# Kernel tuning notes

Hardware: AMD Instinct MI355X
Metric: run time of the kernel (lower is better)

## Reference

```python
import jax, jax.numpy as jnp
import numpy as np

NUM_NODES = 50000
NUM_EDGES = 800000
HIDDEN = 128
HEADS = 8
HEAD_DIM = HIDDEN // HEADS  # 16
FF_HIDDEN = 4 * HIDDEN
LN_EPS = 1e-5


def _xavier(key, shape, gain=0.01):
    fan_out, fan_in = shape
    bound = gain * np.sqrt(6.0 / (fan_in + fan_out))
    return jax.random.uniform(key, shape, jnp.float32, -bound, bound)


def setup_inputs() -> dict:
    key = jax.random.key(0)
    ks = jax.random.split(key, 10)
    x = jax.random.normal(ks[0], (NUM_NODES, HIDDEN), jnp.float32)
    edge_index = jax.random.randint(ks[1], (2, NUM_EDGES), 0, NUM_NODES, jnp.int64)
    return {
        "x": x,
        "edge_index": edge_index,
        "Wq": _xavier(ks[2], (HIDDEN, HIDDEN)),
        "bq": jnp.zeros((HIDDEN,), jnp.float32),
        "Wk": _xavier(ks[3], (HIDDEN, HIDDEN)),
        "bk": jnp.zeros((HIDDEN,), jnp.float32),
        "Wv": _xavier(ks[4], (HIDDEN, HIDDEN)),
        "bv": jnp.zeros((HIDDEN,), jnp.float32),
        "Wo": _xavier(ks[5], (HIDDEN, HIDDEN)),
        "bo": jnp.zeros((HIDDEN,), jnp.float32),
        "W1": _xavier(ks[6], (FF_HIDDEN, HIDDEN)),
        "b1": jnp.zeros((FF_HIDDEN,), jnp.float32),
        "W2": _xavier(ks[7], (HIDDEN, FF_HIDDEN)),
        "b2": jnp.zeros((HIDDEN,), jnp.float32),
        "g1": jnp.ones((HIDDEN,), jnp.float32),
        "be1": jnp.zeros((HIDDEN,), jnp.float32),
        "g2": jnp.ones((HIDDEN,), jnp.float32),
        "be2": jnp.zeros((HIDDEN,), jnp.float32),
    }


def _layernorm(v, g, b):
    mu = jnp.mean(v, axis=-1, keepdims=True)
    var = jnp.mean(jnp.square(v - mu), axis=-1, keepdims=True)
    return (v - mu) * jax.lax.rsqrt(var + LN_EPS) * g + b


def _forward(x, edge_index, Wq, bq, Wk, bk, Wv, bv, Wo, bo, W1, b1, W2, b2, g1, be1, g2, be2):
    src = edge_index[0]  # key/value side (_j)
    dst = edge_index[1]  # query side (_i), aggregation index
    scale = 1.0 / np.sqrt(HEAD_DIM)

    # Euclidean manifold: GeometricLinear == plain linear
    q = (x @ Wq.T + bq).reshape(NUM_NODES, HEADS, HEAD_DIM)
    k = (x @ Wk.T + bk).reshape(NUM_NODES, HEADS, HEAD_DIM)
    v = (x @ Wv.T + bv).reshape(NUM_NODES, HEADS, HEAD_DIM)

    # per-edge attention scores [E, H]
    alpha = jnp.einsum('ehd,ehd->eh', q[dst], k[src]) * scale
    # segment softmax over destination nodes
    m = jax.ops.segment_max(alpha, dst, num_segments=NUM_NODES)  # [N, H]
    ea = jnp.exp(alpha - m[dst])
    denom = jax.ops.segment_sum(ea, dst, num_segments=NUM_NODES)  # [N, H]
    alpha = ea / (denom[dst] + 1e-16)

    # scatter-add weighted values -> [N, H, D]
    agg = jax.ops.segment_sum(v[src] * alpha[..., None], dst, num_segments=NUM_NODES)
    att = agg.reshape(NUM_NODES, HIDDEN) @ Wo.T + bo

    # residual + norm1 (Euclidean)
    h = _layernorm(x + att, g1, be1)

    # feed-forward: fc1 -> exact GELU -> fc2
    ff = (jax.nn.gelu(h @ W1.T + b1, approximate=False)) @ W2.T + b2

    # residual + norm2
    return _layernorm(h + ff, g2, be2)


def reference(x, edge_index, Wq, bq, Wk, bk, Wv, bv, Wo, bo, W1, b1, W2, b2, g1, be1, g2, be2):
    return _forward(x, edge_index, Wq, bq, Wk, bk, Wv, bv, Wo, bo, W1, b1, W2, b2, g1, be1, g2, be2)
```

## Files before the change

kernel.cpp:

```cpp
#include <hip/hip_runtime.h>
#include <math.h>

#define N_HEADS 8
#define HEAD_DIM 16
#define HID 128
#define QKV_ROWB 512

typedef unsigned short ushort_t;
typedef __attribute__((ext_vector_type(8))) short short8;
typedef __attribute__((ext_vector_type(4))) float floatx4;
typedef __attribute__((ext_vector_type(2))) float f32x2;

#define KV_SCALE 64.0f
#define KV_INV_SCALE 0.015625f

#define W2_SCALE 65536.0f
#define A1_SCALE 512.0f
#define FF2_DESCALE (1.0f / 33554432.0f)

#define COUNT_BLOCKS 2048
#define SCAT_BLOCKS 2048

__device__ __forceinline__ ushort_t f2bf(float f) {
    unsigned u = __float_as_uint(f);
    unsigned r = (u + 0x7FFFu + ((u >> 16) & 1u)) >> 16;
    return (ushort_t)r;
}
__device__ __forceinline__ float bf2f(ushort_t u) {
    return __uint_as_float(((unsigned)u) << 16);
}

__device__ __forceinline__ float gelu_f(float x) {
    float z = fabsf(x) * 0.70710678118654752f;
    float t = 1.0f / (1.0f + 0.3275911f * z);
    float y = t * (0.254829592f + t * (-0.284496736f + t * (1.421413741f
            + t * (-1.453152027f + t * 1.061405429f))));
    float e = 1.0f - y * __expf(-z * z);
    e = copysignf(e, x);
    return 0.5f * x * (1.0f + e);
}

__global__ __launch_bounds__(256)
void prep_count_kernel(const float* __restrict__ x,
                 const float* __restrict__ Wq, const float* __restrict__ Wk,
                 const float* __restrict__ Wv, const float* __restrict__ Wo,
                 const float* __restrict__ W1, const float* __restrict__ W2,
                 const float* __restrict__ bq, const float* __restrict__ bk,
                 const float* __restrict__ bv,
                 const int* __restrict__ dst, int* __restrict__ cnt,
                 int* __restrict__ rank, int E, int N,
                 ushort_t* __restrict__ xfrag, ushort_t* __restrict__ wofrag,
                 ushort_t* __restrict__ wqkvf,
                 ushort_t* __restrict__ w1frag,
                 unsigned char* __restrict__ w2frag8,
                 float* __restrict__ bqkv, int xchunks)
{
    if (blockIdx.x < COUNT_BLOCKS) {
        int coh = blockIdx.x & 7;
        int bc  = blockIdx.x >> 3;
        int rr  = (N + 7) >> 3;
        int nlo = coh * rr;
        int nhi = nlo + rr; if (nhi > N) nhi = N;
        const int stride = (COUNT_BLOCKS >> 3) * 256;
        for (int e = bc * 256 + threadIdx.x; e < E; e += stride) {
            int d = dst[e];
            if (d >= nlo && d < nhi) rank[e] = atomicAdd(&cnt[d], 1);
        }
        return;
    }
    int i = (blockIdx.x - COUNT_BLOCKS) * 256 + threadIdx.x;
    if (i < xchunks) {
        int t16 = i >> 8;
        int rem = i & 255;
        int lane = rem & 63;
        int row = t16 * 16 + (lane & 15);
        int k   = (rem >> 6) * 32 + (lane >> 4) * 8;
        const float* s = x + (size_t)row * HID + k;
        short8 v;
#pragma unroll
        for (int e = 0; e < 8; ++e) v[e] = (short)f2bf(s[e]);
        *(short8*)(xfrag + (size_t)i * 8) = v;
        return;
    }
    int j = i - xchunks;
    if (j < 2048) {
        int lane = j & 63, tk = j >> 6;
        int t16 = tk >> 2, kst = tk & 3;
        int row = t16 * 16 + (lane & 15);
        int kb  = kst * 32 + (lane >> 4) * 8;
        const float* s = Wo + (size_t)row * HID + kb;
        short8 v;
#pragma unroll
        for (int e = 0; e < 8; ++e) v[e] = (short)f2bf(s[e]);
        *(short8*)(wofrag + (size_t)j * 8) = v;
        return;
    }
    int b = j - 2048;
    if (b < 6144) {
        int w = b >> 11;
        int rem = b & 2047;
        int t16 = rem >> 8;
        int rem2 = rem & 255;
        int lane = rem2 & 63;
        int row = t16 * 16 + (lane & 15);
        int k   = ((rem2 >> 6) & 3) * 32 + (lane >> 4) * 8;
        const float* W = (w == 0) ? Wq : (w == 1) ? Wk : Wv;
        const float* s = W + (size_t)row * HID + k;
        short8 v;
#pragma unroll
        for (int e = 0; e < 8; ++e) v[e] = (short)f2bf(s[e]);
        *(short8*)(wqkvf + (size_t)b * 8) = v;
        return;
    }
    int c = b - 6144;
    if (c < 8192) {
        int lane = c & 63, tk = c >> 6;
        int t16 = tk >> 2, kst = tk & 3;
        int row = t16 * 16 + (lane & 15);
        int kb  = kst * 32 + (lane >> 4) * 8;
        const float* s = W1 + (size_t)row * HID + kb;
        short8 v;
#pragma unroll
        for (int e = 0; e < 8; ++e) v[e] = (short)f2bf(s[e]);
        *(short8*)(w1frag + (size_t)c * 8) = v;
        return;
    }
    int c2 = c - 8192;
    if (c2 < 8192) {
        int lane = c2 & 63, tk = c2 >> 6;
        int t16 = tk >> 4, kst = tk & 15;
        int row = t16 * 16 + (lane & 15);
        int kb  = kst * 32 + (lane >> 4) * 8;
        const float* s = W2 + (size_t)row * 512 + kb;
        unsigned u0 = 0, u1 = 0;
        u0 = __builtin_amdgcn_cvt_pk_fp8_f32(s[0]*W2_SCALE, s[1]*W2_SCALE, u0, false);
        u0 = __builtin_amdgcn_cvt_pk_fp8_f32(s[2]*W2_SCALE, s[3]*W2_SCALE, u0, true);
        u1 = __builtin_amdgcn_cvt_pk_fp8_f32(s[4]*W2_SCALE, s[5]*W2_SCALE, u1, false);
        u1 = __builtin_amdgcn_cvt_pk_fp8_f32(s[6]*W2_SCALE, s[7]*W2_SCALE, u1, true);
        uint2 o; o.x = u0; o.y = u1;
        *(uint2*)(w2frag8 + (size_t)c2 * 8) = o;
        return;
    }
    int d = c2 - 8192;
    if (d < 384) {
        bqkv[d] = (d < 128) ? bq[d] : (d < 256) ? bk[d - 128] : bv[d - 256];
    }
}

__global__ __launch_bounds__(256)
void scan1_kernel(const int* __restrict__ cnt, int* __restrict__ parts, int N)
{
    __shared__ int sd[256];
    int t = threadIdx.x;
    int base = blockIdx.x * 1024 + t * 4;
    int s = 0;
#pragma unroll
    for (int j = 0; j < 4; ++j) if (base + j < N) s += cnt[base + j];
    sd[t] = s; __syncthreads();
    for (int off = 128; off; off >>= 1) {
        if (t < off) sd[t] += sd[t + off];
        __syncthreads();
    }
    if (t == 0) parts[blockIdx.x] = sd[0];
}

__global__ __launch_bounds__(256)
void scan2_kernel(const int* __restrict__ parts, int* __restrict__ poff, int nb)
{
    __shared__ int sd[256];
    int t = threadIdx.x;
    int v = (t < nb) ? parts[t] : 0;
    sd[t] = v; __syncthreads();
    for (int off = 1; off < 256; off <<= 1) {
        int u = (t >= off) ? sd[t - off] : 0;
        __syncthreads();
        sd[t] += u;
        __syncthreads();
    }
    if (t < nb) poff[t] = sd[t] - v;
}

__global__ __launch_bounds__(256)
void scan3_kernel(const int* __restrict__ cnt, const int* __restrict__ poff,
                  int* __restrict__ rp, int N)
{
    __shared__ int sd[256];
    int t = threadIdx.x;
    int base = blockIdx.x * 1024 + t * 4;
    int v0 = (base + 0 < N) ? cnt[base + 0] : 0;
    int v1 = (base + 1 < N) ? cnt[base + 1] : 0;
    int v2 = (base + 2 < N) ? cnt[base + 2] : 0;
    int v3 = (base + 3 < N) ? cnt[base + 3] : 0;
    int s = v0 + v1 + v2 + v3;
    sd[t] = s; __syncthreads();
    for (int off = 1; off < 256; off <<= 1) {
        int u = (t >= off) ? sd[t - off] : 0;
        __syncthreads();
        sd[t] += u;
        __syncthreads();
    }
    int o = poff[blockIdx.x] + sd[t] - s;
    if (base + 0 < N) rp[base + 0] = o;
    if (base + 1 < N) rp[base + 1] = o + v0;
    if (base + 2 < N) rp[base + 2] = o + v0 + v1;
    if (base + 3 < N) rp[base + 3] = o + v0 + v1 + v2;
}

__global__ __launch_bounds__(256)
void scatter_qkv_kernel(const int* __restrict__ src, const int* __restrict__ dst,
                 const int* __restrict__ rp, const int* __restrict__ rank,
                 int* __restrict__ ssrc, int E, int N,
                 const ushort_t* __restrict__ xfrag,
                 const ushort_t* __restrict__ wqkvf,
                 const float* __restrict__ bqkv,
                 ushort_t* __restrict__ qkvb, int nt16, int nxq)
{
    __shared__ __align__(16) ushort_t sT[4][16 * 136];

    if (blockIdx.x < SCAT_BLOCKS) {
        int coh = blockIdx.x & 7;
        int bc  = blockIdx.x >> 3;
        int rr  = (N + 7) >> 3;
        int nlo = coh * rr;
        int nhi = nlo + rr; if (nhi > N) nhi = N;
        const int stride = (SCAT_BLOCKS >> 3) * 256;
        for (int e = bc * 256 + threadIdx.x; e < E; e += stride) {
            int d = dst[e];
            if (d >= nlo && d < nhi) ssrc[rp[d] + rank[e]] = src[e];
        }
        return;
    }

    const int qi = blockIdx.x - SCAT_BLOCKS;
    const int y  = qi / nxq;
    const int bx = qi - y * nxq;
    const int wave = threadIdx.x >> 6, lane = threadIdx.x & 63;
    const int l15 = lane & 15, l4 = lane >> 4;
    const int gt0 = bx * 8 + wave * 2;
    const int gt0c = (gt0 < nt16) ? gt0 : nt16 - 1;
    const int gt1c = (gt0 + 1 < nt16) ? gt0 + 1 : nt16 - 1;

    floatx4 acc[2][8];
#pragma unroll
    for (int i = 0; i < 2; ++i)
#pragma unroll
        for (int j = 0; j < 8; ++j) acc[i][j] = (floatx4)(0.f);

    const ushort_t* wf = wqkvf + (size_t)y * 16384;
#pragma unroll
    for (int kst = 0; kst < 4; ++kst) {
        short8 a0 = *(const short8*)&xfrag[(((size_t)gt0c * 4 + kst) * 64 + lane) * 8];
        short8 a1 = *(const short8*)&xfrag[(((size_t)gt1c * 4 + kst) * 64 + lane) * 8];
        short8 bv[8];
#pragma unroll
        for (int j = 0; j < 8; ++j)
            bv[j] = *(const short8*)&wf[(((size_t)j * 4 + kst) * 64 + lane) * 8];
#pragma unroll
        for (int j = 0; j < 8; ++j) {
            acc[0][j] = __builtin_amdgcn_mfma_f32_16x16x32_bf16(a0, bv[j], acc[0][j], 0, 0, 0);
            acc[1][j] = __builtin_amdgcn_mfma_f32_16x16x32_bf16(a1, bv[j], acc[1][j], 0, 0, 0);
        }
    }

    float bb[8];
#pragma unroll
    for (int j = 0; j < 8; ++j) bb[j] = bqkv[y * 128 + j * 16 + l15];

#pragma unroll
    for (int i = 0; i < 2; ++i) {
        const int gt = gt0 + i;
#pragma unroll
        for (int j = 0; j < 8; ++j)
#pragma unroll
            for (int r = 0; r < 4; ++r) {
                float v = acc[i][j][r] + bb[j];
                if (y) v *= KV_SCALE;
                sT[wave][(l4 * 4 + r) * 136 + j * 16 + l15] = f2bf(v);
            }
        if (gt < nt16) {
            if (y == 0) {
#pragma unroll
                for (int c = 0; c < 4; ++c) {
                    int ch = l4 * 4 + c;
                    *(short8*)&qkvb[(size_t)(gt * 16 + l15) * 256 + ch * 8] =
                        *(const short8*)&sT[wave][l15 * 136 + ch * 8];
                }
            } else {
                const int koff = (y - 1) * 8;
#pragma unroll
                for (int c = 0; c < 4; ++c) {
                    int ch = l4 * 4 + c;
                    short8 s = *(const short8*)&sT[wave][l15 * 136 + ch * 8];
                    unsigned u0 = 0, u1 = 0;
                    u0 = __builtin_amdgcn_cvt_pk_fp8_f32(
                             bf2f((ushort_t)s[0]), bf2f((ushort_t)s[1]), u0, false);
                    u0 = __builtin_amdgcn_cvt_pk_fp8_f32(
                             bf2f((ushort_t)s[2]), bf2f((ushort_t)s[3]), u0, true);
                    u1 = __builtin_amdgcn_cvt_pk_fp8_f32(
                             bf2f((ushort_t)s[4]), bf2f((ushort_t)s[5]), u1, false);
                    u1 = __builtin_amdgcn_cvt_pk_fp8_f32(
                             bf2f((ushort_t)s[6]), bf2f((ushort_t)s[7]), u1, true);
                    uint2 o; o.x = u0; o.y = u1;
                    *(uint2*)((char*)qkvb + (size_t)(gt * 16 + l15) * QKV_ROWB
                              + 256 + ch * 16 + koff) = o;
                }
            }
        }
    }
}

__global__ __launch_bounds__(256)
void wow_kernel(const ushort_t* __restrict__ aggfrag,
                const ushort_t* __restrict__ wofrag,
                const float* __restrict__ bo,
                const float* __restrict__ x,
                const float* __restrict__ g, const float* __restrict__ be,
                ushort_t* __restrict__ hb, ushort_t* __restrict__ hfrag, int M)
{
    __shared__ __align__(16) ushort_t sT[4][16 * 136];
    const int wave = threadIdx.x >> 6, lane = threadIdx.x & 63;
    const int t32 = blockIdx.x * 4 + wave;
    const int nt32 = (M + 31) / 32;
    if (t32 >= nt32) return;
    const int nt16 = (M + 15) / 16;
    const int gt0 = t32 * 2;
    const int gt1c = (gt0 + 1 < nt16) ? gt0 + 1 : nt16 - 1;
    const int l15 = lane & 15, l4 = lane >> 4;

    floatx4 acc[2][8];
#pragma unroll
    for (int i = 0; i < 2; ++i)
#pragma unroll
        for (int j = 0; j < 8; ++j) acc[i][j] = (floatx4)(0.f);

#pragma unroll
    for (int kst = 0; kst < 4; ++kst) {
        short8 a0 = *(const short8*)&aggfrag[(((size_t)gt0  * 4 + kst) * 64 + lane) * 8];
        short8 a1 = *(const short8*)&aggfrag[(((size_t)gt1c * 4 + kst) * 64 + lane) * 8];
        short8 bv[8];
#pragma unroll
        for (int j = 0; j < 8; ++j)
            bv[j] = *(const short8*)&wofrag[(((size_t)j * 4 + kst) * 64 + lane) * 8];
#pragma unroll
        for (int j = 0; j < 8; ++j) {
            acc[0][j] = __builtin_amdgcn_mfma_f32_16x16x32_bf16(a0, bv[j], acc[0][j], 0, 0, 0);
            acc[1][j] = __builtin_amdgcn_mfma_f32_16x16x32_bf16(a1, bv[j], acc[1][j], 0, 0, 0);
        }
    }

    float bov[8], gv[8], bev[8];
#pragma unroll
    for (int j = 0; j < 8; ++j) {
        int oc = j * 16 + l15;
        bov[j] = bo[oc]; gv[j] = g[oc]; bev[j] = be[oc];
    }

#pragma unroll
    for (int i = 0; i < 2; ++i) {
        const int gt = gt0 + i;
        const int rb = gt * 16;
#pragma unroll
        for (int j = 0; j < 8; ++j) {
            int oc = j * 16 + l15;
#pragma unroll
            for (int r = 0; r < 4; ++r) {
                int row = rb + l4 * 4 + r;
                int rc = (row < M) ? row : M - 1;
                acc[i][j][r] += bov[j] + x[(size_t)rc * HID + oc];
            }
        }
#pragma unroll
        for (int r = 0; r < 4; ++r) {
            float s1 = 0.f, s2 = 0.f;
#pragma unroll
            for (int j = 0; j < 8; ++j) {
                s1 += acc[i][j][r];
                s2 += acc[i][j][r] * acc[i][j][r];
            }
            s1 += __shfl_xor(s1, 1); s1 += __shfl_xor(s1, 2);
            s1 += __shfl_xor(s1, 4); s1 += __shfl_xor(s1, 8);
            s2 += __shfl_xor(s2, 1); s2 += __shfl_xor(s2, 2);
            s2 += __shfl_xor(s2, 4); s2 += __shfl_xor(s2, 8);
            float mu = s1 * (1.f / 128.f);
            float var = s2 * (1.f / 128.f) - mu * mu;
            float rstd = rsqrtf(var + 1e-5f);
#pragma unroll
            for (int j = 0; j < 8; ++j) {
                float v = (acc[i][j][r] - mu) * rstd * gv[j] + bev[j];
                sT[wave][(l4 * 4 + r) * 136 + j * 16 + l15] = f2bf(v);
            }
        }
        if (gt < nt16) {
#pragma unroll
            for (int c = 0; c < 4; ++c) {
                int ch = l4 * 4 + c;
                *(short8*)&hb[(size_t)(gt * 16 + l15) * HID + ch * 8] =
                    *(const short8*)&sT[wave][l15 * 136 + ch * 8];
            }
#pragma unroll
            for (int q = 0; q < 4; ++q)
                *(short8*)&hfrag[(((size_t)gt * 4 + q) * 64 + lane) * 8] =
                    *(const short8*)&sT[wave][l15 * 136 + q * 32 + l4 * 8];
        }
    }
}

__global__ __launch_bounds__(256)
void ff1w_kernel(const ushort_t* __restrict__ hfrag,
                 const ushort_t* __restrict__ w1frag,
                 const float* __restrict__ b1,
                 unsigned char* __restrict__ a1img, int M)
{
    __shared__ __align__(16) ushort_t sT[4][16 * 136];
    const int wave = threadIdx.x >> 6, lane = threadIdx.x & 63;
    const int cg = wave;
    const int nt16 = (M + 15) / 16;
    const int gt0 = blockIdx.x * 2;
    const int gt1 = gt0 + 1;
    const int gt1c = (gt1 < nt16) ? gt1 : nt16 - 1;
    const int l15 = lane & 15, l4 = lane >> 4;

    floatx4 acc[2][8];
#pragma unroll
    for (int i = 0; i < 2; ++i)
#pragma unroll
        for (int j = 0; j < 8; ++j) acc[i][j] = (floatx4)(0.f);

#pragma unroll
    for (int kst = 0; kst < 4; ++kst) {
        short8 a0 = *(const short8*)&hfrag[(((size_t)gt0  * 4 + kst) * 64 + lane) * 8];
        short8 a1 = *(const short8*)&hfrag[(((size_t)gt1c * 4 + kst) * 64 + lane) * 8];
        short8 bv[8];
#pragma unroll
        for (int j = 0; j < 8; ++j)
            bv[j] = *(const short8*)&w1frag[((((size_t)cg * 8 + j) * 4 + kst) * 64 + lane) * 8];
#pragma unroll
        for (int j = 0; j < 8; ++j) {
            acc[0][j] = __builtin_amdgcn_mfma_f32_16x16x32_bf16(a0, bv[j], acc[0][j], 0, 0, 0);
            acc[1][j] = __builtin_amdgcn_mfma_f32_16x16x32_bf16(a1, bv[j], acc[1][j], 0, 0, 0);
        }
    }

    float b1v[8];
#pragma unroll
    for (int j = 0; j < 8; ++j) b1v[j] = b1[cg * 128 + j * 16 + l15];

#pragma unroll
    for (int i = 0; i < 2; ++i) {
        const int gt = i ? gt1 : gt0;
#pragma unroll
        for (int j = 0; j < 8; ++j)
#pragma unroll
            for (int r = 0; r < 4; ++r)
                sT[wave][(l4 * 4 + r) * 136 + j * 16 + l15] =
                    f2bf(gelu_f(acc[i][j][r] + b1v[j]));
        if (gt < nt16) {
#pragma unroll
            for (int q = 0; q < 4; ++q) {
                float v[8];
#pragma unroll
                for (int e = 0; e < 8; ++e)
                    v[e] = bf2f(sT[wave][l15 * 136 + q * 32 + l4 * 8 + e]) * A1_SCALE;
                unsigned u0 = 0, u1 = 0;
                u0 = __builtin_amdgcn_cvt_pk_fp8_f32(v[0], v[1], u0, false);
                u0 = __builtin_amdgcn_cvt_pk_fp8_f32(v[2], v[3], u0, true);
                u1 = __builtin_amdgcn_cvt_pk_fp8_f32(v[4], v[5], u1, false);
                u1 = __builtin_amdgcn_cvt_pk_fp8_f32(v[6], v[7], u1, true);
                uint2 o; o.x = u0; o.y = u1;
                *(uint2*)(a1img + (((size_t)gt * 16 + cg * 4 + q) * 64 + lane) * 8) = o;
            }
        }
    }
}

__global__ __launch_bounds__(256)
void ff2w_kernel(const unsigned char* __restrict__ a1img,
                 const unsigned char* __restrict__ w2frag8,
                 const ushort_t* __restrict__ hb,
                 const float* __restrict__ b2,
                 const float* __restrict__ g, const float* __restrict__ be,
                 float* __restrict__ out, int M)
{
    const int wave = threadIdx.x >> 6, lane = threadIdx.x & 63;
    const int t32 = blockIdx.x * 4 + wave;
    const int nt32 = (M + 31) / 32;
    if (t32 >= nt32) return;
    const int nt16 = (M + 15) / 16;
    const int gt0 = t32 * 2;
    const int gt1c = (gt0 + 1 < nt16) ? gt0 + 1 : nt16 - 1;
    const int l15 = lane & 15, l4 = lane >> 4;

    floatx4 acc[2][8];
#pragma unroll
    for (int i = 0; i < 2; ++i)
#pragma unroll
        for (int j = 0; j < 8; ++j) acc[i][j] = (floatx4)(0.f);

#pragma unroll
    for (int kst = 0; kst < 16; ++kst) {
        long a0 = *(const long*)(a1img + (((size_t)gt0  * 16 + kst) * 64 + lane) * 8);
        long a1 = *(const long*)(a1img + (((size_t)gt1c * 16 + kst) * 64 + lane) * 8);
        long bv[8];
#pragma unroll
        for (int j = 0; j < 8; ++j)
            bv[j] = *(const long*)(w2frag8 + (((size_t)j * 16 + kst) * 64 + lane) * 8);
#pragma unroll
        for (int j = 0; j < 8; ++j) {
            acc[0][j] = __builtin_amdgcn_mfma_f32_16x16x32_fp8_fp8(a0, bv[j], acc[0][j], 0, 0, 0);
            acc[1][j] = __builtin_amdgcn_mfma_f32_16x16x32_fp8_fp8(a1, bv[j], acc[1][j], 0, 0, 0);
        }
    }

    float b2v[8], gv[8], bev[8];
#pragma unroll
    for (int j = 0; j < 8; ++j) {
        int oc = j * 16 + l15;
        b2v[j] = b2[oc]; gv[j] = g[oc]; bev[j] = be[oc];
    }

#pragma unroll
    for (int i = 0; i < 2; ++i) {
        const int rb = (t32 * 2 + i) * 16;
#pragma unroll
        for (int j = 0; j < 8; ++j) {
            int oc = j * 16 + l15;
#pragma unroll
            for (int r = 0; r < 4; ++r) {
                int row = rb + l4 * 4 + r;
                int rc = (row < M) ? row : M - 1;
                acc[i][j][r] = acc[i][j][r] * FF2_DESCALE + b2v[j]
                             + bf2f(hb[(size_t)rc * HID + oc]);
            }
        }
#pragma unroll
        for (int r = 0; r < 4; ++r) {
            float s1 = 0.f, s2 = 0.f;
#pragma unroll
            for (int j = 0; j < 8; ++j) {
                s1 += acc[i][j][r];
                s2 += acc[i][j][r] * acc[i][j][r];
            }
            s1 += __shfl_xor(s1, 1); s1 += __shfl_xor(s1, 2);
            s1 += __shfl_xor(s1, 4); s1 += __shfl_xor(s1, 8);
            s2 += __shfl_xor(s2, 1); s2 += __shfl_xor(s2, 2);
            s2 += __shfl_xor(s2, 4); s2 += __shfl_xor(s2, 8);
            float mu = s1 * (1.f / 128.f);
            float var = s2 * (1.f / 128.f) - mu * mu;
            float rstd = rsqrtf(var + 1e-5f);
            int row = rb + l4 * 4 + r;
            if (row < M) {
#pragma unroll
                for (int j = 0; j < 8; ++j)
                    out[(size_t)row * HID + j * 16 + l15] =
                        (acc[i][j][r] - mu) * rstd * gv[j] + bev[j];
            }
        }
    }
}

__global__ __launch_bounds__(256)
void attn_fused_kernel(const ushort_t* __restrict__ qkvb, const int* __restrict__ rp,
                       const int* __restrict__ ssrc, ushort_t* __restrict__ aggfrag,
                       int N, int E)
{
    int wave = threadIdx.x >> 6, lane = threadIdx.x & 63;
    int n = blockIdx.x * 4 + wave;
    if (n >= N) return;
    int grp = lane >> 4;
    int cb  = (lane & 15) * 16;
    const char* base = (const char*)qkvb;

    short8 qv = *(const short8*)(base + n * QKV_ROWB + cb);
    float q[8];
#pragma unroll
    for (int j = 0; j < 8; ++j) q[j] = bf2f((ushort_t)qv[j]) * (0.25f / KV_SCALE);

    int r0 = rp[n];
    int r1 = (n + 1 < N) ? rp[n + 1] : E;
    float acc[8] = {0.f, 0.f, 0.f, 0.f, 0.f, 0.f, 0.f, 0.f};
    float l = 0.f;

    int r = r0;
    for (; r + 8 <= r1; r += 8) {
        int s0 = ssrc[r + grp];
        int s1 = ssrc[r + 4 + grp];
        uint4 kv0 = *(const uint4*)(base + s0 * QKV_ROWB + 256 + cb);
        uint4 kv1 = *(const uint4*)(base + s1 * QKV_ROWB + 256 + cb);

        f32x2 a0 = __builtin_amdgcn_cvt_pk_f32_fp8(kv0.x, false);
        f32x2 a1 = __builtin_amdgcn_cvt_pk_f32_fp8(kv0.x, true);
        f32x2 a2 = __builtin_amdgcn_cvt_pk_f32_fp8(kv0.y, false);
        f32x2 a3 = __builtin_amdgcn_cvt_pk_f32_fp8(kv0.y, true);
        f32x2 b0 = __builtin_amdgcn_cvt_pk_f32_fp8(kv1.x, false);
        f32x2 b1 = __builtin_amdgcn_cvt_pk_f32_fp8(kv1.x, true);
        f32x2 b2 = __builtin_amdgcn_cvt_pk_f32_fp8(kv1.y, false);
        f32x2 b3 = __builtin_amdgcn_cvt_pk_f32_fp8(kv1.y, true);

        float p0 = 0.f, p1 = 0.f;
        p0 = fmaf(q[0], a0.x, p0); p0 = fmaf(q[1], a0.y, p0);
        p0 = fmaf(q[2], a1.x, p0); p0 = fmaf(q[3], a1.y, p0);
        p0 = fmaf(q[4], a2.x, p0); p0 = fmaf(q[5], a2.y, p0);
        p0 = fmaf(q[6], a3.x, p0); p0 = fmaf(q[7], a3.y, p0);
        p1 = fmaf(q[0], b0.x, p1); p1 = fmaf(q[1], b0.y, p1);
        p1 = fmaf(q[2], b1.x, p1); p1 = fmaf(q[3], b1.y, p1);
        p1 = fmaf(q[4], b2.x, p1); p1 = fmaf(q[5], b2.y, p1);
        p1 = fmaf(q[6], b3.x, p1); p1 = fmaf(q[7], b3.y, p1);

        p0 += __shfl_xor(p0, 1);
        p1 += __shfl_xor(p1, 1);
        float e0 = __expf(p0), e1 = __expf(p1);
        l += e0 + e1;

        f32x2 v0 = __builtin_amdgcn_cvt_pk_f32_fp8(kv0.z, false);
        f32x2 v1 = __builtin_amdgcn_cvt_pk_f32_fp8(kv0.z, true);
        f32x2 v2 = __builtin_amdgcn_cvt_pk_f32_fp8(kv0.w, false);
        f32x2 v3 = __builtin_amdgcn_cvt_pk_f32_fp8(kv0.w, true);
        f32x2 w0 = __builtin_amdgcn_cvt_pk_f32_fp8(kv1.z, false);
        f32x2 w1 = __builtin_amdgcn_cvt_pk_f32_fp8(kv1.z, true);
        f32x2 w2 = __builtin_amdgcn_cvt_pk_f32_fp8(kv1.w, false);
        f32x2 w3 = __builtin_amdgcn_cvt_pk_f32_fp8(kv1.w, true);

        acc[0] = fmaf(e0, v0.x, acc[0]); acc[1] = fmaf(e0, v0.y, acc[1]);
        acc[2] = fmaf(e0, v1.x, acc[2]); acc[3] = fmaf(e0, v1.y, acc[3]);
        acc[4] = fmaf(e0, v2.x, acc[4]); acc[5] = fmaf(e0, v2.y, acc[5]);
        acc[6] = fmaf(e0, v3.x, acc[6]); acc[7] = fmaf(e0, v3.y, acc[7]);
        acc[0] = fmaf(e1, w0.x, acc[0]); acc[1] = fmaf(e1, w0.y, acc[1]);
        acc[2] = fmaf(e1, w1.x, acc[2]); acc[3] = fmaf(e1, w1.y, acc[3]);
        acc[4] = fmaf(e1, w2.x, acc[4]); acc[5] = fmaf(e1, w2.y, acc[5]);
        acc[6] = fmaf(e1, w3.x, acc[6]); acc[7] = fmaf(e1, w3.y, acc[7]);
    }
    for (; r < r1; r += 4) {
        int e = r + grp;
        int s = ssrc[(e < r1) ? e : r0];
        uint4 kv = *(const uint4*)(base + s * QKV_ROWB + 256 + cb);
        f32x2 a0 = __builtin_amdgcn_cvt_pk_f32_fp8(kv.x, false);
        f32x2 a1 = __builtin_amdgcn_cvt_pk_f32_fp8(kv.x, true);
        f32x2 a2 = __builtin_amdgcn_cvt_pk_f32_fp8(kv.y, false);
        f32x2 a3 = __builtin_amdgcn_cvt_pk_f32_fp8(kv.y, true);
        float p = 0.f;
        p = fmaf(q[0], a0.x, p); p = fmaf(q[1], a0.y, p);
        p = fmaf(q[2], a1.x, p); p = fmaf(q[3], a1.y, p);
        p = fmaf(q[4], a2.x, p); p = fmaf(q[5], a2.y, p);
        p = fmaf(q[6], a3.x, p); p = fmaf(q[7], a3.y, p);
        p += __shfl_xor(p, 1);
        float ea = (e < r1) ? __expf(p) : 0.f;
        l += ea;
        f32x2 v0 = __builtin_amdgcn_cvt_pk_f32_fp8(kv.z, false);
        f32x2 v1 = __builtin_amdgcn_cvt_pk_f32_fp8(kv.z, true);
        f32x2 v2 = __builtin_amdgcn_cvt_pk_f32_fp8(kv.w, false);
        f32x2 v3 = __builtin_amdgcn_cvt_pk_f32_fp8(kv.w, true);
        acc[0] = fmaf(ea, v0.x, acc[0]); acc[1] = fmaf(ea, v0.y, acc[1]);
        acc[2] = fmaf(ea, v1.x, acc[2]); acc[3] = fmaf(ea, v1.y, acc[3]);
        acc[4] = fmaf(ea, v2.x, acc[4]); acc[5] = fmaf(ea, v2.y, acc[5]);
        acc[6] = fmaf(ea, v3.x, acc[6]); acc[7] = fmaf(ea, v3.y, acc[7]);
    }

#pragma unroll
    for (int j = 0; j < 8; ++j) {
        acc[j] += __shfl_xor(acc[j], 16);
        acc[j] += __shfl_xor(acc[j], 32);
    }
    l += __shfl_xor(l, 16);
    l += __shfl_xor(l, 32);
    float inv = KV_INV_SCALE / (l + 1e-16f);
    if (grp == 0) {
        short8 o;
#pragma unroll
        for (int j = 0; j < 8; ++j) o[j] = (short)f2bf(acc[j] * inv);
        int t16 = n >> 4, kst = lane >> 2;
        int lp = (n & 15) + ((lane & 3) << 4);
        *(short8*)&aggfrag[(((size_t)t16 * 4 + kst) * 64 + lp) * 8] = o;
    }
}

extern "C" void kernel_launch(void* const* d_in, const int* in_sizes, int n_in,
                              void* d_out, int out_size, void* d_ws, size_t ws_size,
                              hipStream_t stream)
{
    const float* x  = (const float*)d_in[0];
    const int*   ei = (const int*)d_in[1];
    const float* Wq = (const float*)d_in[2];
    const float* bq = (const float*)d_in[3];
    const float* Wk = (const float*)d_in[4];
    const float* bk = (const float*)d_in[5];
    const float* Wv = (const float*)d_in[6];
    const float* bv = (const float*)d_in[7];
    const float* Wo = (const float*)d_in[8];
    const float* bo = (const float*)d_in[9];
    const float* W1 = (const float*)d_in[10];
    const float* b1 = (const float*)d_in[11];
    const float* W2 = (const float*)d_in[12];
    const float* b2 = (const float*)d_in[13];
    const float* g1 = (const float*)d_in[14];
    const float* be1= (const float*)d_in[15];
    const float* g2 = (const float*)d_in[16];
    const float* be2= (const float*)d_in[17];
    float* out = (float*)d_out;

    const int N = in_sizes[0] / HID;
    const int E = in_sizes[1] / 2;
    const int* srcp = ei;
    const int* dstp = ei + E;

    const size_t NH = (size_t)N * HID;
    float* wsf = (float*)d_ws;

    const int nt16 = (N + 15) / 16;
    const int nt32 = (N + 31) / 32;

    ushort_t* xfrag   = (ushort_t*)wsf;
    ushort_t* qkvb    = (ushort_t*)(wsf + NH / 2);
    ushort_t* hfrag   = (ushort_t*)(wsf + NH + NH / 2);
    ushort_t* aggfrag = (ushort_t*)(wsf + 2 * NH);
    ushort_t* hb      = (ushort_t*)wsf;
    unsigned char* a1img = (unsigned char*)(wsf + NH / 2);

    ushort_t* U       = (ushort_t*)(wsf + 2 * NH + NH / 2);
    ushort_t* wofrag  = U;
    ushort_t* wqkvf   = U + 16384;
    ushort_t* w1frag  = U + 65536;
    unsigned char* w2frag8 = (unsigned char*)(U + 131072);
    float*    bqkv = (float*)(w2frag8 + 65536);
    int*      rp   = (int*)(bqkv + 384);
    int*      cnt  = rp + (N + 1);
    int*      poff = cnt + N;
    int*      parts= poff + 256;
    int*      ssrc = parts + 256;
    int*      rank = ssrc + E;

    hipMemsetAsync(cnt, 0, N * sizeof(int), stream);
    const int xchunks = nt16 * 256;
    const int ptot = xchunks + 2048 + 6144 + 8192 + 8192 + 384;
    const int prepB = (ptot + 255) / 256;
    prep_count_kernel<<<COUNT_BLOCKS + prepB, 256, 0, stream>>>(
        x, Wq, Wk, Wv, Wo, W1, W2, bq, bk, bv,
        dstp, cnt, rank, E, N,
        xfrag, wofrag, wqkvf, w1frag, w2frag8, bqkv, xchunks);

    const int nb = (N + 1023) / 1024;
    scan1_kernel<<<nb, 256, 0, stream>>>(cnt, parts, N);
    scan2_kernel<<<1, 256, 0, stream>>>(parts, poff, nb);
    scan3_kernel<<<nb, 256, 0, stream>>>(cnt, poff, rp, N);

    const int nxq = (nt16 + 7) / 8;
    scatter_qkv_kernel<<<SCAT_BLOCKS + nxq * 3, 256, 0, stream>>>(
        srcp, dstp, rp, rank, ssrc, E, N,
        xfrag, wqkvf, bqkv, qkvb, nt16, nxq);

    attn_fused_kernel<<<(N + 3) / 4, 256, 0, stream>>>(
        qkvb, rp, ssrc, aggfrag, N, E);

    wow_kernel<<<(nt32 + 3) / 4, 256, 0, stream>>>(
        aggfrag, wofrag, bo, x, g1, be1, hb, hfrag, N);

    ff1w_kernel<<<nt32, 256, 0, stream>>>(hfrag, w1frag, b1, a1img, N);

    ff2w_kernel<<<(nt32 + 3) / 4, 256, 0, stream>>>(
        a1img, w2frag8, hb, b2, g2, be2, out, N);
}
```

Baseline: 298.0 us.

## Fuse output projection, LayerNorm, FFN and final LayerNorm into one kernel

Merges the Wo projection + residual + LN1 kernel, the FF1+GELU kernel and the FF2 + residual + LN2 kernel into a single per-wave kernel. Each wave keeps its 32-row tile of h in LDS, computes the 512-wide hidden layer in four 128-column chunks, quantises each chunk to fp8 in LDS and accumulates FF2 immediately. This removes the global round-trips of hb, hfrag and the fp8 activation image, plus two launches. In exchange it uses much more LDS per block and more accumulator registers, which can lower occupancy, and FF1 now runs on one wave per row tile rather than four waves sharing it.

```diff
diff --git a/kernel.cpp b/kernel.cpp
--- a/kernel.cpp
+++ b/kernel.cpp
@@ -310,14 +310,21 @@
 }
 
 __global__ __launch_bounds__(256)
-void wow_kernel(const ushort_t* __restrict__ aggfrag,
-                const ushort_t* __restrict__ wofrag,
-                const float* __restrict__ bo,
-                const float* __restrict__ x,
-                const float* __restrict__ g, const float* __restrict__ be,
-                ushort_t* __restrict__ hb, ushort_t* __restrict__ hfrag, int M)
+void ffall_kernel(const ushort_t* __restrict__ aggfrag,
+                  const ushort_t* __restrict__ wofrag,
+                  const float* __restrict__ bo,
+                  const float* __restrict__ x,
+                  const float* __restrict__ g1, const float* __restrict__ be1,
+                  const ushort_t* __restrict__ w1frag,
+                  const float* __restrict__ b1,
+                  const unsigned char* __restrict__ w2frag8,
+                  const float* __restrict__ b2,
+                  const float* __restrict__ g2, const float* __restrict__ be2,
+                  float* __restrict__ out, int M)
 {
-    __shared__ __align__(16) ushort_t sT[4][16 * 136];
+    __shared__ __align__(16) ushort_t sH[4][32 * 136];
+    __shared__ __align__(16) unsigned char sA[4][32 * 136];
+    __shared__ __align__(16) ushort_t sS[4][16 * 136];
     const int wave = threadIdx.x >> 6, lane = threadIdx.x & 63;
     const int t32 = blockIdx.x * 4 + wave;
     const int nt32 = (M + 31) / 32;
@@ -332,7 +339,6 @@
     for (int i = 0; i < 2; ++i)
 #pragma unroll
         for (int j = 0; j < 8; ++j) acc[i][j] = (floatx4)(0.f);
-
 #pragma unroll
     for (int kst = 0; kst < 4; ++kst) {
         short8 a0 = *(const short8*)&aggfrag[(((size_t)gt0  * 4 + kst) * 64 + lane) * 8];
@@ -348,211 +354,160 @@
         }
     }
 
-    float bov[8], gv[8], bev[8];
-#pragma unroll
-    for (int j = 0; j < 8; ++j) {
-        int oc = j * 16 + l15;
-        bov[j] = bo[oc]; gv[j] = g[oc]; bev[j] = be[oc];
-    }
-
-#pragma unroll
-    for (int i = 0; i < 2; ++i) {
-        const int gt = gt0 + i;
-        const int rb = gt * 16;
+    {
+        float bov[8], gv[8], bev[8];
 #pragma unroll
         for (int j = 0; j < 8; ++j) {
             int oc = j * 16 + l15;
+            bov[j] = bo[oc]; gv[j] = g1[oc]; bev[j] = be1[oc];
+        }
+#pragma unroll
+        for (int i = 0; i < 2; ++i) {
+            const int rb = (gt0 + i) * 16;
+#pragma unroll
+            for (int j = 0; j < 8; ++j) {
+                int oc = j * 16 + l15;
+#pragma unroll
+                for (int r = 0; r < 4; ++r) {
+                    int row = rb + l4 * 4 + r;
+                    int rc = (row < M) ? row : M - 1;
+                    acc[i][j][r] += bov[j] + x[(size_t)rc * HID + oc];
+                }
+            }
 #pragma unroll
             for (int r = 0; r < 4; ++r) {
-                int row = rb + l4 * 4 + r;
-                int rc = (row < M) ? row : M - 1;
-                acc[i][j][r] += bov[j] + x[(size_t)rc * HID + oc];
-            }
-        }
-#pragma unroll
-        for (int r = 0; r < 4; ++r) {
-            float s1 = 0.f, s2 = 0.f;
+                float s1 = 0.f, s2 = 0.f;
+#pragma unroll
+                for (int j = 0; j < 8; ++j) {
+                    s1 += acc[i][j][r];
+                    s2 += acc[i][j][r] * acc[i][j][r];
+                }
+                s1 += __shfl_xor(s1, 1); s1 += __shfl_xor(s1, 2);
+                s1 += __shfl_xor(s1, 4); s1 += __shfl_xor(s1, 8);
+                s2 += __shfl_xor(s2, 1); s2 += __shfl_xor(s2, 2);
+                s2 += __shfl_xor(s2, 4); s2 += __shfl_xor(s2, 8);
+                float mu = s1 * (1.f / 128.f);
+                float var = s2 * (1.f / 128.f) - mu * mu;
+                float rstd = rsqrtf(var + 1e-5f);
+#pragma unroll
+                for (int j = 0; j < 8; ++j) {
+                    float v = (acc[i][j][r] - mu) * rstd * gv[j] + bev[j];
+                    sH[wave][(i * 16 + l4 * 4 + r) * 136 + j * 16 + l15] = f2bf(v);
+                }
+            }
+        }
+    }
+
+    floatx4 acc2[2][8];
+#pragma unroll
+    for (int i = 0; i < 2; ++i)
+#pragma unroll
+        for (int j = 0; j < 8; ++j) acc2[i][j] = (floatx4)(0.f);
+
+    for (int fc = 0; fc < 4; ++fc) {
+        floatx4 acc1[2][8];
+#pragma unroll
+        for (int i = 0; i < 2; ++i)
+#pragma unroll
+            for (int j = 0; j < 8; ++j) acc1[i][j] = (floatx4)(0.f);
+#pragma unroll
+        for (int kst = 0; kst < 4; ++kst) {
+            short8 a0 = *(const short8*)&sH[wave][l15 * 136 + kst * 32 + l4 * 8];
+            short8 a1 = *(const short8*)&sH[wave][(16 + l15) * 136 + kst * 32 + l4 * 8];
+            short8 bv[8];
+#pragma unroll
+            for (int j = 0; j < 8; ++j)
+                bv[j] = *(const short8*)&w1frag[((((size_t)fc * 8 + j) * 4 + kst) * 64 + lane) * 8];
 #pragma unroll
             for (int j = 0; j < 8; ++j) {
-                s1 += acc[i][j][r];
-                s2 += acc[i][j][r] * acc[i][j][r];
-            }
-            s1 += __shfl_xor(s1, 1); s1 += __shfl_xor(s1, 2);
-            s1 += __shfl_xor(s1, 4); s1 += __shfl_xor(s1, 8);
-            s2 += __shfl_xor(s2, 1); s2 += __shfl_xor(s2, 2);
-            s2 += __shfl_xor(s2, 4); s2 += __shfl_xor(s2, 8);
-            float mu = s1 * (1.f / 128.f);
-            float var = s2 * (1.f / 128.f) - mu * mu;
-            float rstd = rsqrtf(var + 1e-5f);
-#pragma unroll
-            for (int j = 0; j < 8; ++j) {
-                float v = (acc[i][j][r] - mu) * rstd * gv[j] + bev[j];
-                sT[wave][(l4 * 4 + r) * 136 + j * 16 + l15] = f2bf(v);
-            }
-        }
-        if (gt < nt16) {
-#pragma unroll
-            for (int c = 0; c < 4; ++c) {
-                int ch = l4 * 4 + c;
-                *(short8*)&hb[(size_t)(gt * 16 + l15) * HID + ch * 8] =
-                    *(const short8*)&sT[wave][l15 * 136 + ch * 8];
-            }
-#pragma unroll
-            for (int q = 0; q < 4; ++q)
-                *(short8*)&hfrag[(((size_t)gt * 4 + q) * 64 + lane) * 8] =
-                    *(const short8*)&sT[wave][l15 * 136 + q * 32 + l4 * 8];
-        }
-    }
-}
-
-__global__ __launch_bounds__(256)
-void ff1w_kernel(const ushort_t* __restrict__ hfrag,
-                 const ushort_t* __restrict__ w1frag,
-                 const float* __restrict__ b1,
-                 unsigned char* __restrict__ a1img, int M)
-{
-    __shared__ __align__(16) ushort_t sT[4][16 * 136];
-    const int wave = threadIdx.x >> 6, lane = threadIdx.x & 63;
-    const int cg = wave;
-    const int nt16 = (M + 15) / 16;
-    const int gt0 = blockIdx.x * 2;
-    const int gt1 = gt0 + 1;
-    const int gt1c = (gt1 < nt16) ? gt1 : nt16 - 1;
-    const int l15 = lane & 15, l4 = lane >> 4;
-
-    floatx4 acc[2][8];
-#pragma unroll
-    for (int i = 0; i < 2; ++i)
-#pragma unroll
-        for (int j = 0; j < 8; ++j) acc[i][j] = (floatx4)(0.f);
-
-#pragma unroll
-    for (int kst = 0; kst < 4; ++kst) {
-        short8 a0 = *(const short8*)&hfrag[(((size_t)gt0  * 4 + kst) * 64 + lane) * 8];
-        short8 a1 = *(const short8*)&hfrag[(((size_t)gt1c * 4 + kst) * 64 + lane) * 8];
-        short8 bv[8];
-#pragma unroll
-        for (int j = 0; j < 8; ++j)
-            bv[j] = *(const short8*)&w1frag[((((size_t)cg * 8 + j) * 4 + kst) * 64 + lane) * 8];
-#pragma unroll
-        for (int j = 0; j < 8; ++j) {
-            acc[0][j] = __builtin_amdgcn_mfma_f32_16x16x32_bf16(a0, bv[j], acc[0][j], 0, 0, 0);
-            acc[1][j] = __builtin_amdgcn_mfma_f32_16x16x32_bf16(a1, bv[j], acc[1][j], 0, 0, 0);
-        }
-    }
-
-    float b1v[8];
-#pragma unroll
-    for (int j = 0; j < 8; ++j) b1v[j] = b1[cg * 128 + j * 16 + l15];
-
-#pragma unroll
-    for (int i = 0; i < 2; ++i) {
-        const int gt = i ? gt1 : gt0;
-#pragma unroll
-        for (int j = 0; j < 8; ++j)
-#pragma unroll
-            for (int r = 0; r < 4; ++r)
-                sT[wave][(l4 * 4 + r) * 136 + j * 16 + l15] =
-                    f2bf(gelu_f(acc[i][j][r] + b1v[j]));
-        if (gt < nt16) {
+                acc1[0][j] = __builtin_amdgcn_mfma_f32_16x16x32_bf16(a0, bv[j], acc1[0][j], 0, 0, 0);
+                acc1[1][j] = __builtin_amdgcn_mfma_f32_16x16x32_bf16(a1, bv[j], acc1[1][j], 0, 0, 0);
+            }
+        }
+        float b1v[8];
+#pragma unroll
+        for (int j = 0; j < 8; ++j) b1v[j] = b1[fc * 128 + j * 16 + l15];
+#pragma unroll
+        for (int i = 0; i < 2; ++i) {
+#pragma unroll
+            for (int j = 0; j < 8; ++j)
+#pragma unroll
+                for (int r = 0; r < 4; ++r)
+                    sS[wave][(l4 * 4 + r) * 136 + j * 16 + l15] =
+                        f2bf(gelu_f(acc1[i][j][r] + b1v[j]));
 #pragma unroll
             for (int q = 0; q < 4; ++q) {
                 float v[8];
 #pragma unroll
                 for (int e = 0; e < 8; ++e)
-                    v[e] = bf2f(sT[wave][l15 * 136 + q * 32 + l4 * 8 + e]) * A1_SCALE;
+                    v[e] = bf2f(sS[wave][l15 * 136 + q * 32 + l4 * 8 + e]) * A1_SCALE;
                 unsigned u0 = 0, u1 = 0;
                 u0 = __builtin_amdgcn_cvt_pk_fp8_f32(v[0], v[1], u0, false);
                 u0 = __builtin_amdgcn_cvt_pk_fp8_f32(v[2], v[3], u0, true);
                 u1 = __builtin_amdgcn_cvt_pk_fp8_f32(v[4], v[5], u1, false);
                 u1 = __builtin_amdgcn_cvt_pk_fp8_f32(v[6], v[7], u1, true);
                 uint2 o; o.x = u0; o.y = u1;
-                *(uint2*)(a1img + (((size_t)gt * 16 + cg * 4 + q) * 64 + lane) * 8) = o;
-            }
-        }
-    }
-}
-
-__global__ __launch_bounds__(256)
-void ff2w_kernel(const unsigned char* __restrict__ a1img,
-                 const unsigned char* __restrict__ w2frag8,
-                 const ushort_t* __restrict__ hb,
-                 const float* __restrict__ b2,
-                 const float* __restrict__ g, const float* __restrict__ be,
-                 float* __restrict__ out, int M)
-{
-    const int wave = threadIdx.x >> 6, lane = threadIdx.x & 63;
-    const int t32 = blockIdx.x * 4 + wave;
-    const int nt32 = (M + 31) / 32;
-    if (t32 >= nt32) return;
-    const int nt16 = (M + 15) / 16;
-    const int gt0 = t32 * 2;
-    const int gt1c = (gt0 + 1 < nt16) ? gt0 + 1 : nt16 - 1;
-    const int l15 = lane & 15, l4 = lane >> 4;
-
-    floatx4 acc[2][8];
-#pragma unroll
-    for (int i = 0; i < 2; ++i)
-#pragma unroll
-        for (int j = 0; j < 8; ++j) acc[i][j] = (floatx4)(0.f);
-
-#pragma unroll
-    for (int kst = 0; kst < 16; ++kst) {
-        long a0 = *(const long*)(a1img + (((size_t)gt0  * 16 + kst) * 64 + lane) * 8);
-        long a1 = *(const long*)(a1img + (((size_t)gt1c * 16 + kst) * 64 + lane) * 8);
-        long bv[8];
-#pragma unroll
-        for (int j = 0; j < 8; ++j)
-            bv[j] = *(const long*)(w2frag8 + (((size_t)j * 16 + kst) * 64 + lane) * 8);
-#pragma unroll
-        for (int j = 0; j < 8; ++j) {
-            acc[0][j] = __builtin_amdgcn_mfma_f32_16x16x32_fp8_fp8(a0, bv[j], acc[0][j], 0, 0, 0);
-            acc[1][j] = __builtin_amdgcn_mfma_f32_16x16x32_fp8_fp8(a1, bv[j], acc[1][j], 0, 0, 0);
-        }
-    }
-
-    float b2v[8], gv[8], bev[8];
-#pragma unroll
-    for (int j = 0; j < 8; ++j) {
-        int oc = j * 16 + l15;
-        b2v[j] = b2[oc]; gv[j] = g[oc]; bev[j] = be[oc];
-    }
-
-#pragma unroll
-    for (int i = 0; i < 2; ++i) {
-        const int rb = (t32 * 2 + i) * 16;
+                *(uint2*)&sA[wave][(i * 16 + l15) * 136 + q * 32 + l4 * 8] = o;
+            }
+        }
+#pragma unroll
+        for (int kst = 0; kst < 4; ++kst) {
+            long a0 = *(const long*)&sA[wave][l15 * 136 + kst * 32 + l4 * 8];
+            long a1 = *(const long*)&sA[wave][(16 + l15) * 136 + kst * 32 + l4 * 8];
+            const int gk = fc * 4 + kst;
+            long bv[8];
+#pragma unroll
+            for (int j = 0; j < 8; ++j)
+                bv[j] = *(const long*)(w2frag8 + (((size_t)j * 16 + gk) * 64 + lane) * 8);
+#pragma unroll
+            for (int j = 0; j < 8; ++j) {
+                acc2[0][j] = __builtin_amdgcn_mfma_f32_16x16x32_fp8_fp8(a0, bv[j], acc2[0][j], 0, 0, 0);
+                acc2[1][j] = __builtin_amdgcn_mfma_f32_16x16x32_fp8_fp8(a1, bv[j], acc2[1][j], 0, 0, 0);
+            }
+        }
+    }
+
+    {
+        float b2v[8], gv[8], bev[8];
 #pragma unroll
         for (int j = 0; j < 8; ++j) {
             int oc = j * 16 + l15;
+            b2v[j] = b2[oc]; gv[j] = g2[oc]; bev[j] = be2[oc];
+        }
+#pragma unroll
+        for (int i = 0; i < 2; ++i) {
+            const int rb = (gt0 + i) * 16;
+#pragma unroll
+            for (int j = 0; j < 8; ++j) {
+                int oc = j * 16 + l15;
+#pragma unroll
+                for (int r = 0; r < 4; ++r) {
+                    acc2[i][j][r] = acc2[i][j][r] * FF2_DESCALE + b2v[j]
+                                  + bf2f(sH[wave][(i * 16 + l4 * 4 + r) * 136 + oc]);
+                }
+            }
 #pragma unroll
             for (int r = 0; r < 4; ++r) {
+                float s1 = 0.f, s2 = 0.f;
+#pragma unroll
+                for (int j = 0; j < 8; ++j) {
+                    s1 += acc2[i][j][r];
+                    s2 += acc2[i][j][r] * acc2[i][j][r];
+                }
+                s1 += __shfl_xor(s1, 1); s1 += __shfl_xor(s1, 2);
+                s1 += __shfl_xor(s1, 4); s1 += __shfl_xor(s1, 8);
+                s2 += __shfl_xor(s2, 1); s2 += __shfl_xor(s2, 2);
+                s2 += __shfl_xor(s2, 4); s2 += __shfl_xor(s2, 8);
+                float mu = s1 * (1.f / 128.f);
+                float var = s2 * (1.f / 128.f) - mu * mu;
+                float rstd = rsqrtf(var + 1e-5f);
                 int row = rb + l4 * 4 + r;
-                int rc = (row < M) ? row : M - 1;
-                acc[i][j][r] = acc[i][j][r] * FF2_DESCALE + b2v[j]
-                             + bf2f(hb[(size_t)rc * HID + oc]);
-            }
-        }
-#pragma unroll
-        for (int r = 0; r < 4; ++r) {
-            float s1 = 0.f, s2 = 0.f;
-#pragma unroll
-            for (int j = 0; j < 8; ++j) {
-                s1 += acc[i][j][r];
-                s2 += acc[i][j][r] * acc[i][j][r];
-            }
-            s1 += __shfl_xor(s1, 1); s1 += __shfl_xor(s1, 2);
-            s1 += __shfl_xor(s1, 4); s1 += __shfl_xor(s1, 8);
-            s2 += __shfl_xor(s2, 1); s2 += __shfl_xor(s2, 2);
-            s2 += __shfl_xor(s2, 4); s2 += __shfl_xor(s2, 8);
-            float mu = s1 * (1.f / 128.f);
-            float var = s2 * (1.f / 128.f) - mu * mu;
-            float rstd = rsqrtf(var + 1e-5f);
-            int row = rb + l4 * 4 + r;
-            if (row < M) {
-#pragma unroll
-                for (int j = 0; j < 8; ++j)
-                    out[(size_t)row * HID + j * 16 + l15] =
-                        (acc[i][j][r] - mu) * rstd * gv[j] + bev[j];
+                if (row < M) {
+#pragma unroll
+                    for (int j = 0; j < 8; ++j)
+                        out[(size_t)row * HID + j * 16 + l15] =
+                            (acc2[i][j][r] - mu) * rstd * gv[j] + bev[j];
+                }
             }
         }
     }
@@ -710,10 +665,7 @@
 
     ushort_t* xfrag   = (ushort_t*)wsf;
     ushort_t* qkvb    = (ushort_t*)(wsf + NH / 2);
-    ushort_t* hfrag   = (ushort_t*)(wsf + NH + NH / 2);
     ushort_t* aggfrag = (ushort_t*)(wsf + 2 * NH);
-    ushort_t* hb      = (ushort_t*)wsf;
-    unsigned char* a1img = (unsigned char*)(wsf + NH / 2);
 
     ushort_t* U       = (ushort_t*)(wsf + 2 * NH + NH / 2);
     ushort_t* wofrag  = U;
@@ -750,11 +702,7 @@
     attn_fused_kernel<<<(N + 3) / 4, 256, 0, stream>>>(
         qkvb, rp, ssrc, aggfrag, N, E);
 
-    wow_kernel<<<(nt32 + 3) / 4, 256, 0, stream>>>(
-        aggfrag, wofrag, bo, x, g1, be1, hb, hfrag, N);
-
-    ff1w_kernel<<<nt32, 256, 0, stream>>>(hfrag, w1frag, b1, a1img, N);
-
-    ff2w_kernel<<<(nt32 + 3) / 4, 256, 0, stream>>>(
-        a1img, w2frag8, hb, b2, g2, be2, out, N);
-}
+    ffall_kernel<<<(nt32 + 3) / 4, 256, 0, stream>>>(
+        aggfrag, wofrag, bo, x, g1, be1,
+        w1frag, b1, w2frag8, b2, g2, be2, out, N);
+}
```

Result: slower. 318.5 us (+6.9%).
